# Optimization experiments

Hardware: AMD Instinct MI355X
Metric: run time of the kernel (lower is better)

The kernel has to match this reference:

```python
import jax, jax.numpy as jnp
import numpy as np

EMBED_DIM = 1024
LN_EPS = 1e-5


def _layernorm(x, w, b):
    m = jnp.mean(x, axis=-1, keepdims=True)
    v = jnp.mean(jnp.square(x - m), axis=-1, keepdims=True)
    return (x - m) * jax.lax.rsqrt(v + LN_EPS) * w + b


def _attention(q, k, v, scale):
    # q: [b, sq, d], k/v: [b, sk, d]
    scores = jnp.einsum('bqd,bkd->bqk', q, k) * scale
    probs = jax.nn.softmax(scores, axis=-1)
    return jnp.einsum('bqk,bkd->bqd', probs, v)


def setup_inputs() -> dict:
    key = jax.random.key(0)
    ks = jax.random.split(key, 16)
    B, SQ, SK, D, H = 8, 577, 13271, EMBED_DIM, 4  # H=int(4.0) per source
    return {
        'input_features': jax.random.normal(ks[0], (B, SK, D), jnp.float32),
        'query_feature': jax.random.normal(ks[1], (B, SQ, D), jnp.float32),
        'norm1_w': jax.random.uniform(ks[2], (D,), jnp.float32, 0.5, 1.5),
        'norm1_b': jax.random.normal(ks[3], (D,), jnp.float32) * 0.1,
        'norm2_w': jax.random.uniform(ks[4], (D,), jnp.float32, 0.5, 1.5),
        'norm2_b': jax.random.normal(ks[5], (D,), jnp.float32) * 0.1,
        'norm3_w': jax.random.uniform(ks[6], (D,), jnp.float32, 0.5, 1.5),
        'norm3_b': jax.random.normal(ks[7], (D,), jnp.float32) * 0.1,
        'gamma1': jax.random.uniform(ks[8], (D,), jnp.float32, 0.5, 1.5),
        'gamma2': jax.random.uniform(ks[9], (D,), jnp.float32, 0.5, 1.5),
        'fc1_w': jax.random.normal(ks[10], (H, D), jnp.float32) * (1.0 / np.sqrt(D)),
        'fc1_b': jax.random.normal(ks[11], (H,), jnp.float32) * 0.01,
        'fc2_w': jax.random.normal(ks[12], (D, H), jnp.float32) * (1.0 / np.sqrt(H)),
        'fc2_b': jax.random.normal(ks[13], (D,), jnp.float32) * 0.01,
    }


def reference(input_features, query_feature, norm1_w, norm1_b, norm2_w, norm2_b,
              norm3_w, norm3_b, gamma1, gamma2, fc1_w, fc1_b, fc2_w, fc2_b):
    scale = EMBED_DIM ** (-0.5)
    norm_X = _layernorm(input_features, norm1_w, norm1_b)
    norm_F_L = _layernorm(query_feature, norm2_w, norm2_b)
    # cross attention: query = last-layer feats, key/value = concat of earlier layers
    attended = _attention(norm_F_L, norm_X, norm_X, scale)
    # MLP with exact-erf GELU (torch nn.GELU default), dropout=0 -> identity
    h = jax.nn.gelu(attended @ fc1_w.T + fc1_b, approximate=False)
    cross_attended = h @ fc2_w.T + fc2_b
    norm_cross = _layernorm(cross_attended, norm3_w, norm3_b)
    self_attended = _attention(norm_cross, norm_cross, norm_cross, scale)
    skip_connect = cross_attended + gamma1 * self_attended
    return norm_F_L + gamma2 * skip_connect
```

## Files before the change

### kernel.cpp

```cpp
#include <hip/hip_runtime.h>
#include <hip/hip_bf16.h>
#include <math.h>

typedef unsigned short u16;
typedef __attribute__((ext_vector_type(4))) unsigned short u16x4;
typedef __attribute__((ext_vector_type(8))) __bf16 bf16x8;
typedef __attribute__((ext_vector_type(4))) float fx4;

#define DEV __device__ __forceinline__

DEV u16 f2bf(float f) {
    unsigned u = __float_as_uint(f);
    u += 0x7fffu + ((u >> 16) & 1u);
    return (u16)(u >> 16);
}

DEV void async_load16(const void* g, void* l) {
    __builtin_amdgcn_global_load_lds(
        (const __attribute__((address_space(1))) void*)g,
        (__attribute__((address_space(3))) void*)l, 16, 0, 0);
}

DEV void block_reduce2(float& a, float& b) {
    #pragma unroll
    for (int o = 32; o; o >>= 1) { a += __shfl_xor(a, o); b += __shfl_xor(b, o); }
    __shared__ float sa[4], sb[4];
    const int lane = threadIdx.x & 63, wv = threadIdx.x >> 6;
    if (lane == 0) { sa[wv] = a; sb[wv] = b; }
    __syncthreads();
    a = sa[0] + sa[1] + sa[2] + sa[3];
    b = sb[0] + sb[1] + sb[2] + sb[3];
    __syncthreads();
}

DEV void xcd_swizzle3(int& bx, int& by, int& bz) {
    const int nx = gridDim.x, ny = gridDim.y;
    const int total = nx * ny * gridDim.z;
    const int lin = blockIdx.x + nx * (blockIdx.y + ny * blockIdx.z);
    if (total & 7) { bx = blockIdx.x; by = blockIdx.y; bz = blockIdx.z; return; }
    const int cpx = total >> 3;
    const int swz = (lin & 7) * cpx + (lin >> 3);
    bx = swz % nx;
    const int r = swz / nx;
    by = r % ny;
    bz = r / ny;
}

__global__ __launch_bounds__(256) void ln_k(
    const float* __restrict__ in, int rows_real,
    const float* __restrict__ w, const float* __restrict__ bias,
    u16* __restrict__ out_bf, float* __restrict__ out_f32, float out_scale)
{
    const int r = blockIdx.x, b = blockIdx.y, tid = threadIdx.x;
    const int rows_pad = gridDim.x;
    const size_t orow = ((size_t)b * rows_pad + r) * 1024 + tid * 4;
    if (r >= rows_real) {
        u16x4 z = {0, 0, 0, 0};
        *(u16x4*)&out_bf[orow] = z;
        if (out_f32) { fx4 zf = {0.f, 0.f, 0.f, 0.f}; *(fx4*)&out_f32[orow] = zf; }
        return;
    }
    const size_t irow = ((size_t)b * rows_real + r) * 1024 + tid * 4;
    fx4 x = *(const fx4*)&in[irow];
    float s1 = x.x + x.y + x.z + x.w;
    float s2 = x.x * x.x + x.y * x.y + x.z * x.z + x.w * x.w;
    block_reduce2(s1, s2);
    float m = s1 * (1.0f / 1024.0f);
    float var = s2 * (1.0f / 1024.0f) - m * m;
    float rs = rsqrtf(var + 1e-5f);
    fx4 wv4 = *(const fx4*)&w[tid * 4];
    fx4 bv4 = *(const fx4*)&bias[tid * 4];
    fx4 y;
    y.x = (x.x - m) * rs * wv4.x + bv4.x;
    y.y = (x.y - m) * rs * wv4.y + bv4.y;
    y.z = (x.z - m) * rs * wv4.z + bv4.z;
    y.w = (x.w - m) * rs * wv4.w + bv4.w;
    u16x4 o = { f2bf(y.x * out_scale), f2bf(y.y * out_scale),
                f2bf(y.z * out_scale), f2bf(y.w * out_scale) };
    *(u16x4*)&out_bf[orow] = o;
    if (out_f32) *(fx4*)&out_f32[orow] = y;
}

template<bool ATOMIC>
DEV void gemm_body(
    const u16* __restrict__ Ab, const u16* __restrict__ Bb, float* __restrict__ Cb,
    int k_begin, int iters, int lda, int ldb, int ldc)
{
    __shared__ u16 lA[2][128 * 32];
    __shared__ u16 lB[2][128 * 32];
    const int lane = threadIdx.x & 63, wv = threadIdx.x >> 6;
    const int wm = (wv >> 1) * 64, wn = (wv & 1) * 64;
    const int frow = lane & 15, quad = lane >> 4;

    fx4 acc[4][4];
    #pragma unroll
    for (int i = 0; i < 4; ++i)
        #pragma unroll
        for (int j = 0; j < 4; ++j) { acc[i][j].x = 0; acc[i][j].y = 0; acc[i][j].z = 0; acc[i][j].w = 0; }

    const int c0 = wv * 64 + lane;
    const int r0a = c0 >> 2, s0 = (c0 & 3) * 8;
    const int c1 = 256 + c0;
    const int r1a = c1 >> 2, s1 = (c1 & 3) * 8;

    auto stage = [&](int buf, int it) {
        const int k0 = k_begin + it * 32;
        async_load16(Ab + (size_t)r0a * lda + k0 + s0, &lA[buf][(wv * 64) * 8]);
        async_load16(Ab + (size_t)r1a * lda + k0 + s1, &lA[buf][(256 + wv * 64) * 8]);
        async_load16(Bb + (size_t)r0a * ldb + k0 + s0, &lB[buf][(wv * 64) * 8]);
        async_load16(Bb + (size_t)r1a * ldb + k0 + s1, &lB[buf][(256 + wv * 64) * 8]);
    };

    stage(0, 0);
    __syncthreads();
    int cur = 0;
    for (int it = 0; it < iters; ++it) {
        if (it + 1 < iters) stage(cur ^ 1, it + 1);
        bf16x8 af[4], bfr[4];
        #pragma unroll
        for (int i = 0; i < 4; ++i) {
            af[i]  = *(const bf16x8*)&lA[cur][(wm + i * 16 + frow) * 32 + quad * 8];
            bfr[i] = *(const bf16x8*)&lB[cur][(wn + i * 16 + frow) * 32 + quad * 8];
        }
        #pragma unroll
        for (int mi = 0; mi < 4; ++mi)
            #pragma unroll
            for (int ni = 0; ni < 4; ++ni)
                acc[mi][ni] = __builtin_amdgcn_mfma_f32_16x16x32_bf16(af[mi], bfr[ni], acc[mi][ni], 0, 0, 0);
        __syncthreads();
        cur ^= 1;
    }

    #pragma unroll
    for (int mi = 0; mi < 4; ++mi) {
        #pragma unroll
        for (int r = 0; r < 4; ++r) {
            const int row = wm + mi * 16 + quad * 4 + r;
            #pragma unroll
            for (int ni = 0; ni < 4; ++ni) {
                const int col = wn + ni * 16 + frow;
                if (ATOMIC) atomicAdd(&Cb[(size_t)row * ldc + col], acc[mi][ni][r]);
                else        __builtin_nontemporal_store(acc[mi][ni][r], &Cb[(size_t)row * ldc + col]);
            }
        }
    }
}

template<int NS>
__global__ __launch_bounds__(256) void gemm_bt_sk(
    const u16* __restrict__ A, const u16* __restrict__ B, float* __restrict__ C,
    int iters_per, int lda, int ldb, int ldc, long As, long Bs, long Cs)
{
    int bx, by, bzz;
    xcd_swizzle3(bx, by, bzz);
    const int bz = bzz / NS, sp = bzz % NS;
    const u16* Ab = A + (size_t)bz * As + (size_t)by * 128 * lda;
    const u16* Bb = B + (size_t)bz * Bs + (size_t)bx * 128 * ldb;
    float* Cb = C + (size_t)bz * Cs + (size_t)by * 128 * ldc + (size_t)bx * 128;
    gemm_body<true>(Ab, Bb, Cb, sp * iters_per * 32, iters_per, lda, ldb, ldc);
}

template<bool ATOMIC>
DEV void gemm256_body(
    const u16* __restrict__ A, const u16* __restrict__ B, float* __restrict__ C,
    int k_begin, int NT, int lda, int ldb, int ldc, int bx, int by, int Mreal)
{
    __shared__ u16 lds[2][4][8192];
    const int tid = threadIdx.x;
    const int lane = tid & 63, wid = tid >> 6;
    const int wr = wid >> 2, wc = wid & 3;
    const int frow = lane & 15, quad = lane >> 4;
    const int sw = (frow & 7) << 4;
    const int csrc = ((lane & 7) ^ ((lane >> 3) & 7)) * 8;
    const int by256 = by * 256, bx256 = bx * 256;
    const int mclamp = Mreal - 1;

    fx4 acc[8][4];
    #pragma unroll
    for (int i = 0; i < 8; ++i)
        #pragma unroll
        for (int j = 0; j < 4; ++j) { acc[i][j].x = 0; acc[i][j].y = 0; acc[i][j].z = 0; acc[i][j].w = 0; }

    auto stageA = [&](int buf, int half, int ktile) {
        const int kcol = k_begin + ktile * 64;
        #pragma unroll
        for (int j = 0; j < 2; ++j) {
            int grow = by256 + half * 128 + (wid * 2 + j) * 8 + (lane >> 3);
            if (grow > mclamp) grow = mclamp;
            async_load16(A + (size_t)grow * lda + kcol + csrc,
                         &lds[buf][half][(wid * 2 + j) * 512]);
        }
    };
    auto stageB = [&](int buf, int half, int ktile) {
        const int kcol = k_begin + ktile * 64;
        #pragma unroll
        for (int j = 0; j < 2; ++j) {
            const int grow = bx256 + half * 128 + (wid * 2 + j) * 8 + (lane >> 3);
            async_load16(B + (size_t)grow * ldb + kcol + csrc,
                         &lds[buf][2 + half][(wid * 2 + j) * 512]);
        }
    };

#define DO_PHASE(MQ, NQ, STAGE_STMT, WAITN)                                              \
    {                                                                                    \
        STAGE_STMT;                                                                      \
        __builtin_amdgcn_sched_barrier(0);                                               \
        asm volatile("s_waitcnt vmcnt(" #WAITN ")" ::: "memory");                        \
        __builtin_amdgcn_s_barrier();                                                    \
        __builtin_amdgcn_sched_barrier(0);                                               \
        const char* pa = (const char*)&lds[cur][MQ][0];                                  \
        const char* pb = (const char*)&lds[cur][2 + NQ][0];                              \
        bf16x8 av[4][2], bv[2][2];                                                       \
        _Pragma("unroll")                                                                \
        for (int f = 0; f < 4; ++f) {                                                    \
            const int row = wr * 64 + f * 16 + frow;                                     \
            _Pragma("unroll")                                                            \
            for (int ks = 0; ks < 2; ++ks)                                               \
                av[f][ks] = *(const bf16x8*)(pa + row * 128 + ((((ks * 4 + quad) << 4)) ^ sw)); \
        }                                                                                \
        _Pragma("unroll")                                                                \
        for (int gg = 0; gg < 2; ++gg) {                                                 \
            const int col = wc * 32 + gg * 16 + frow;                                    \
            _Pragma("unroll")                                                            \
            for (int ks = 0; ks < 2; ++ks)                                               \
                bv[gg][ks] = *(const bf16x8*)(pb + col * 128 + ((((ks * 4 + quad) << 4)) ^ sw)); \
        }                                                                                \
        __builtin_amdgcn_s_setprio(1);                                                   \
        _Pragma("unroll")                                                                \
        for (int f = 0; f < 4; ++f)                                                      \
            _Pragma("unroll")                                                            \
            for (int gg = 0; gg < 2; ++gg)                                               \
                _Pragma("unroll")                                                        \
                for (int ks = 0; ks < 2; ++ks)                                           \
                    acc[MQ * 4 + f][NQ * 2 + gg] = __builtin_amdgcn_mfma_f32_16x16x32_bf16( \
                        av[f][ks], bv[gg][ks], acc[MQ * 4 + f][NQ * 2 + gg], 0, 0, 0);   \
        __builtin_amdgcn_s_setprio(0);                                                   \
    }

    stageA(0, 0, 0);
    stageB(0, 0, 0);
    stageB(0, 1, 0);
    stageA(0, 1, 0);
    stageA(1, 0, 1);

    int cur = 0;
    for (int t = 0; t <= NT - 2; ++t) {
        const int nxt = cur ^ 1;
        DO_PHASE(0, 0, stageB(nxt, 0, t + 1), 8)
        DO_PHASE(0, 1, stageB(nxt, 1, t + 1), 8)
        DO_PHASE(1, 0, stageA(nxt, 1, t + 1), 8)
        DO_PHASE(1, 1, if (t + 2 < NT) stageA(cur, 0, t + 2), 8)
        cur = nxt;
    }
    DO_PHASE(0, 0, (void)0, 4)
    DO_PHASE(0, 1, (void)0, 2)
    DO_PHASE(1, 0, (void)0, 0)
    DO_PHASE(1, 1, (void)0, 0)
#undef DO_PHASE

    #pragma unroll
    for (int mf = 0; mf < 8; ++mf) {
        const int rowb = (mf >> 2) * 128 + wr * 64 + (mf & 3) * 16 + quad * 4;
        #pragma unroll
        for (int r = 0; r < 4; ++r) {
            const int grow = by256 + rowb + r;
            if (grow < Mreal) {
                #pragma unroll
                for (int nf = 0; nf < 4; ++nf) {
                    const int gcol = bx256 + (nf >> 1) * 128 + wc * 32 + (nf & 1) * 16 + frow;
                    if (ATOMIC) atomicAdd(&C[(size_t)grow * ldc + gcol], acc[mf][nf][r]);
                    else __builtin_nontemporal_store(acc[mf][nf][r], &C[(size_t)grow * ldc + gcol]);
                }
            }
        }
    }
}

__global__ __launch_bounds__(512, 2) void gemm256_qk(
    const u16* __restrict__ A, const u16* __restrict__ B, float* __restrict__ C,
    int NT, int lda, int ldb, int ldc, long As, long Bs, long Cs, int Mreal)
{
    const int lin = blockIdx.x + gridDim.x * (blockIdx.y + gridDim.y * blockIdx.z);
    const int per_bx = gridDim.y * gridDim.z;
    const int bx = lin / per_bx, rem = lin % per_bx;
    const int by = rem % gridDim.y, bz = rem / gridDim.y;
    gemm256_body<false>(A + (size_t)bz * As, B + (size_t)bz * Bs, C + (size_t)bz * Cs,
                        0, NT, lda, ldb, ldc, bx, by, Mreal);
}

template<int NS>
__global__ __launch_bounds__(512, 2) void gemm256_sk(
    const u16* __restrict__ A, const u16* __restrict__ B, float* __restrict__ C,
    int NT_per, int lda, int ldb, int ldc, long As, long Bs, long Cs, int Mreal)
{
    int bx, by, bzz;
    xcd_swizzle3(bx, by, bzz);
    const int bz = bzz / NS, sp = bzz % NS;
    gemm256_body<true>(A + (size_t)bz * As, B + (size_t)bz * Bs, C + (size_t)bz * Cs,
                       sp * NT_per * 64, NT_per, lda, ldb, ldc, bx, by, Mreal);
}

template<int EPT4>
__global__ __launch_bounds__(256) void softmax_k(
    const float* __restrict__ S, u16* __restrict__ P,
    int n_real, int n_pad, float scale, long Ss, long Ps)
{
    const int tid = threadIdx.x;
    const float* Sr = S + (size_t)blockIdx.y * Ss + (size_t)blockIdx.x * n_pad;
    u16* Pr = P + (size_t)blockIdx.y * Ps + (size_t)blockIdx.x * n_pad;
    fx4 v[EPT4];
    float mx = -INFINITY;
    #pragma unroll
    for (int i = 0; i < EPT4; ++i) {
        const int base = (i * 256 + tid) * 4;
        fx4 s;
        if (base < n_pad) s = *(const fx4*)&Sr[base];
        else { s.x = -INFINITY; s.y = -INFINITY; s.z = -INFINITY; s.w = -INFINITY; }
        s.x = (base + 0 < n_real) ? s.x * scale : -INFINITY;
        s.y = (base + 1 < n_real) ? s.y * scale : -INFINITY;
        s.z = (base + 2 < n_real) ? s.z * scale : -INFINITY;
        s.w = (base + 3 < n_real) ? s.w * scale : -INFINITY;
        v[i] = s;
        mx = fmaxf(mx, fmaxf(fmaxf(s.x, s.y), fmaxf(s.z, s.w)));
    }
    #pragma unroll
    for (int o = 32; o; o >>= 1) mx = fmaxf(mx, __shfl_xor(mx, o));
    __shared__ float sm[4];
    const int lane = tid & 63, wvi = tid >> 6;
    if (lane == 0) sm[wvi] = mx;
    __syncthreads();
    mx = fmaxf(fmaxf(sm[0], sm[1]), fmaxf(sm[2], sm[3]));
    __syncthreads();
    float sum = 0.f;
    #pragma unroll
    for (int i = 0; i < EPT4; ++i) {
        fx4 e;
        e.x = __expf(v[i].x - mx); e.y = __expf(v[i].y - mx);
        e.z = __expf(v[i].z - mx); e.w = __expf(v[i].w - mx);
        v[i] = e;
        sum += e.x + e.y + e.z + e.w;
    }
    #pragma unroll
    for (int o = 32; o; o >>= 1) sum += __shfl_xor(sum, o);
    if (lane == 0) sm[wvi] = sum;
    __syncthreads();
    sum = sm[0] + sm[1] + sm[2] + sm[3];
    const float inv = 1.0f / sum;
    #pragma unroll
    for (int i = 0; i < EPT4; ++i) {
        const int base = (i * 256 + tid) * 4;
        if (base < n_pad) {
            u16x4 o = { f2bf(v[i].x * inv), f2bf(v[i].y * inv),
                        f2bf(v[i].z * inv), f2bf(v[i].w * inv) };
            *(u16x4*)&Pr[base] = o;
        }
    }
}

__global__ __launch_bounds__(256) void transpose_k(
    const u16* __restrict__ in, u16* __restrict__ out,
    int in_rows, int in_cols, long is, long os)
{
    __shared__ u16 t[64][68];
    const int b = blockIdx.z;
    const u16* I = in + (size_t)b * is;
    u16* O = out + (size_t)b * os;
    const int c0 = blockIdx.x * 64, r0 = blockIdx.y * 64;
    const int cx = threadIdx.x & 15, ry = threadIdx.x >> 4;
    u16x4 a[4];
    #pragma unroll
    for (int k = 0; k < 4; ++k)
        a[k] = *(const u16x4*)&I[(size_t)(r0 + 4 * ry + k) * in_cols + c0 + 4 * cx];
    #pragma unroll
    for (int e = 0; e < 4; ++e) {
        u16x4 o = { a[0][e], a[1][e], a[2][e], a[3][e] };
        *(u16x4*)&t[4 * cx + e][4 * ry] = o;
    }
    __syncthreads();
    #pragma unroll
    for (int k = 0; k < 4; ++k) {
        const int oc = 4 * ry + k;
        *(u16x4*)&O[(size_t)(c0 + oc) * in_rows + r0 + 4 * cx] =
            *(const u16x4*)&t[oc][4 * cx];
    }
}

__global__ __launch_bounds__(256) void mlp_ln_k(
    const float* __restrict__ att, const float* __restrict__ w1, const float* __restrict__ b1,
    const float* __restrict__ w2, const float* __restrict__ b2,
    const float* __restrict__ w3, const float* __restrict__ b3,
    float* __restrict__ ca, u16* __restrict__ nc, int rows_real)
{
    const int q = blockIdx.x, b = blockIdx.y, tid = threadIdx.x;
    const size_t row = ((size_t)b * gridDim.x + q) * 1024 + tid * 4;
    if (q >= rows_real) {
        fx4 zf = {0.f, 0.f, 0.f, 0.f}; u16x4 z = {0, 0, 0, 0};
        *(fx4*)&ca[row] = zf;
        *(u16x4*)&nc[row] = z;
        return;
    }
    fx4 x = *(const fx4*)&att[row];
    float p[4];
    #pragma unroll
    for (int j = 0; j < 4; ++j) {
        fx4 wj = *(const fx4*)&w1[j * 1024 + tid * 4];
        p[j] = x.x * wj.x + x.y * wj.y + x.z * wj.z + x.w * wj.w;
        #pragma unroll
        for (int o = 32; o; o >>= 1) p[j] += __shfl_xor(p[j], o);
    }
    __shared__ float sh[4][4];
    const int lane = tid & 63, wvi = tid >> 6;
    if (lane == 0) { sh[wvi][0] = p[0]; sh[wvi][1] = p[1]; sh[wvi][2] = p[2]; sh[wvi][3] = p[3]; }
    __syncthreads();
    float h[4];
    #pragma unroll
    for (int j = 0; j < 4; ++j) {
        float s = sh[0][j] + sh[1][j] + sh[2][j] + sh[3][j] + b1[j];
        h[j] = 0.5f * s * (1.0f + erff(s * 0.70710678118f));
    }
    float v[4]; float s1 = 0.f, s2 = 0.f;
    #pragma unroll
    for (int e = 0; e < 4; ++e) {
        const int d = tid * 4 + e;
        fx4 wd = *(const fx4*)&w2[d * 4];
        float t = h[0] * wd.x + h[1] * wd.y + h[2] * wd.z + h[3] * wd.w + b2[d];
        v[e] = t; s1 += t; s2 += t * t;
    }
    block_reduce2(s1, s2);
    const float m = s1 * (1.0f / 1024.0f);
    const float var = s2 * (1.0f / 1024.0f) - m * m;
    const float rs = rsqrtf(var + 1e-5f);
    fx4 cav = {v[0], v[1], v[2], v[3]};
    *(fx4*)&ca[row] = cav;
    fx4 w3v = *(const fx4*)&w3[tid * 4], b3v = *(const fx4*)&b3[tid * 4];
    u16x4 o = { f2bf((v[0] - m) * rs * w3v.x + b3v.x), f2bf((v[1] - m) * rs * w3v.y + b3v.y),
                f2bf((v[2] - m) * rs * w3v.z + b3v.z), f2bf((v[3] - m) * rs * w3v.w + b3v.w) };
    *(u16x4*)&nc[row] = o;
}

__global__ __launch_bounds__(256) void final_k(
    const float* __restrict__ nF, const float* __restrict__ ca,
    const float* __restrict__ att2, const float* __restrict__ g1,
    const float* __restrict__ g2, float* __restrict__ out, int sq, int sqp)
{
    const int q = blockIdx.x, b = blockIdx.y, tid = threadIdx.x;
    const size_t wrow = ((size_t)b * sqp + q) * 1024 + tid * 4;
    const size_t orow = ((size_t)b * sq + q) * 1024 + tid * 4;
    fx4 nf = *(const fx4*)&nF[wrow];
    fx4 c  = *(const fx4*)&ca[wrow];
    fx4 a2 = *(const fx4*)&att2[wrow];
    fx4 G1 = *(const fx4*)&g1[tid * 4];
    fx4 G2 = *(const fx4*)&g2[tid * 4];
    fx4 r;
    r.x = nf.x + G2.x * (c.x + G1.x * a2.x);
    r.y = nf.y + G2.y * (c.y + G1.y * a2.y);
    r.z = nf.z + G2.z * (c.z + G1.z * a2.z);
    r.w = nf.w + G2.w * (c.w + G1.w * a2.w);
    *(fx4*)&out[orow] = r;
}

extern "C" void kernel_launch(void* const* d_in, const int* in_sizes, int n_in,
                              void* d_out, int out_size, void* d_ws, size_t ws_size,
                              hipStream_t stream) {
    const float* x_in = (const float*)d_in[0];
    const float* q_in = (const float*)d_in[1];
    const float* n1w = (const float*)d_in[2];
    const float* n1b = (const float*)d_in[3];
    const float* n2w = (const float*)d_in[4];
    const float* n2b = (const float*)d_in[5];
    const float* n3w = (const float*)d_in[6];
    const float* n3b = (const float*)d_in[7];
    const float* g1  = (const float*)d_in[8];
    const float* g2  = (const float*)d_in[9];
    const float* w1  = (const float*)d_in[10];
    const float* b1  = (const float*)d_in[11];
    const float* w2  = (const float*)d_in[12];
    const float* b2  = (const float*)d_in[13];
    float* out = (float*)d_out;

    const int B = 8, SQ = 577, SK = 13271, D = 1024;
    const int SQP = 640, SKP = 13312;
    const float scale = 0.03125f;

    char* ws = (char*)d_ws;
    size_t off = 0;
    auto alloc = [&](size_t n) { size_t o = off; off = (off + n + 255) & ~(size_t)255; return o; };
    u16*   Xn   = (u16*)  (ws + alloc((size_t)B * SKP * D * 2));
    u16*   Xt   = (u16*)  (ws + alloc((size_t)B * D * SKP * 2));
    u16*   Qb   = (u16*)  (ws + alloc((size_t)B * SQP * D * 2));
    float* nF   = (float*)(ws + alloc((size_t)B * SQP * D * 4));
    u16*   P    = (u16*)  (ws + alloc((size_t)B * SQP * SKP * 2));
    float* att  = (float*)(ws + alloc((size_t)B * SQP * D * 4));
    float* CA   = (float*)(ws + alloc((size_t)B * SQP * D * 4));
    u16*   NC   = (u16*)  (ws + alloc((size_t)B * SQP * D * 2));
    u16*   NCt  = (u16*)  (ws + alloc((size_t)B * D * SQP * 2));
    float* S2   = (float*)(ws + alloc((size_t)B * SQP * SQP * 4));
    u16*   P2   = (u16*)  (ws + alloc((size_t)B * SQP * SQP * 2));
    float* att2 = (float*)(ws + alloc((size_t)B * SQP * D * 4));
    const size_t perS1 = (size_t)SQP * SKP * 4;
    size_t room = (ws_size > off) ? (ws_size - off) / perS1 : 1;
    int g = (int)(room < 1 ? 1 : (room > 8 ? 8 : room));
    float* S1 = (float*)(ws + off);
    (void)in_sizes; (void)n_in; (void)out_size;

    ln_k<<<dim3(SKP, B), 256, 0, stream>>>(x_in, SK, n1w, n1b, Xn, nullptr, 1.0f);
    ln_k<<<dim3(SQP, B), 256, 0, stream>>>(q_in, SQ, n2w, n2b, Qb, nF, scale);

    transpose_k<<<dim3(D / 64, SKP / 64, B), 256, 0, stream>>>(
        Xn, Xt, SKP, D, (long)SKP * D, (long)SKP * D);

    for (int b = 0; b < B; b += g) {
        const int nb = (B - b) < g ? (B - b) : g;
        gemm256_qk<<<dim3(SKP / 256, 3, nb), 512, 0, stream>>>(
            Qb + (size_t)b * SQP * D, Xn + (size_t)b * SKP * D, S1,
            D / 64, D, D, SKP, (long)SQP * D, (long)SKP * D, (long)SQP * SKP, SQP);
        softmax_k<13><<<dim3(SQP, nb), 256, 0, stream>>>(
            S1, P + (size_t)b * SQP * SKP, SK, SKP, 1.0f,
            (long)SQP * SKP, (long)SQP * SKP);
    }

    hipMemsetAsync(att, 0, (size_t)B * SQP * D * 4, stream);
    gemm256_sk<8><<<dim3(D / 256, 3, B * 8), 512, 0, stream>>>(
        P, Xt, att, (SKP / 64) / 8, SKP, SKP, D,
        (long)SQP * SKP, (long)D * SKP, (long)SQP * D, SQP);

    mlp_ln_k<<<dim3(SQP, B), 256, 0, stream>>>(att, w1, b1, w2, b2, n3w, n3b, CA, NC, SQ);

    transpose_k<<<dim3(D / 64, SQP / 64, B), 256, 0, stream>>>(
        NC, NCt, SQP, D, (long)SQP * D, (long)SQP * D);
    hipMemsetAsync(S2, 0, (size_t)B * SQP * SQP * 4, stream);
    gemm_bt_sk<2><<<dim3(SQP / 128, SQP / 128, B * 2), 256, 0, stream>>>(
        NC, NC, S2, 16, D, D, SQP,
        (long)SQP * D, (long)SQP * D, (long)SQP * SQP);
    softmax_k<1><<<dim3(SQP, B), 256, 0, stream>>>(
        S2, P2, SQ, SQP, scale, (long)SQP * SQP, (long)SQP * SQP);
    hipMemsetAsync(att2, 0, (size_t)B * SQP * D * 4, stream);
    gemm_bt_sk<4><<<dim3(D / 128, SQP / 128, B * 4), 256, 0, stream>>>(
        P2, NCt, att2, 5, SQP, SQP, D,
        (long)SQP * SQP, (long)D * SQP, (long)SQP * D);

    final_k<<<dim3(SQ, B), 256, 0, stream>>>(nF, CA, att2, g1, g2, out, SQ, SQP);
}
```

Before: 1.321 ms.

## Use one wave per row in layernorm, plain GEMM stores, smaller S1 batch group

Rewrites the layernorm kernel so each 64-lane wave handles a full 1024-wide row with shuffle reductions, replacing the block-wide LDS reduction and its barriers. GEMM epilogues switch from nontemporal stores to normal stores, so the score matrices can stay in cache for the following softmax. The batch group size for the QK/softmax loop is capped at 4 instead of 8, shrinking the S1 working set so it is more likely to fit in cache, at the cost of more kernel launches.

```diff
diff --git a/kernel.cpp b/kernel.cpp
--- a/kernel.cpp
+++ b/kernel.cpp
@@ -46,39 +46,52 @@
     bz = r / ny;
 }
 
-__global__ __launch_bounds__(256) void ln_k(
-    const float* __restrict__ in, int rows_real,
+__global__ __launch_bounds__(256) void ln_wave_k(
+    const float* __restrict__ in, int rows_real, int rows_pad,
     const float* __restrict__ w, const float* __restrict__ bias,
     u16* __restrict__ out_bf, float* __restrict__ out_f32, float out_scale)
 {
-    const int r = blockIdx.x, b = blockIdx.y, tid = threadIdx.x;
-    const int rows_pad = gridDim.x;
-    const size_t orow = ((size_t)b * rows_pad + r) * 1024 + tid * 4;
+    const int wv = threadIdx.x >> 6, lane = threadIdx.x & 63;
+    const int r = blockIdx.x * 4 + wv, b = blockIdx.y;
+    const size_t orow = ((size_t)b * rows_pad + r) * 1024 + lane * 4;
     if (r >= rows_real) {
         u16x4 z = {0, 0, 0, 0};
-        *(u16x4*)&out_bf[orow] = z;
-        if (out_f32) { fx4 zf = {0.f, 0.f, 0.f, 0.f}; *(fx4*)&out_f32[orow] = zf; }
+        fx4 zf = {0.f, 0.f, 0.f, 0.f};
+        #pragma unroll
+        for (int c = 0; c < 4; ++c) {
+            *(u16x4*)&out_bf[orow + c * 256] = z;
+            if (out_f32) *(fx4*)&out_f32[orow + c * 256] = zf;
+        }
         return;
     }
-    const size_t irow = ((size_t)b * rows_real + r) * 1024 + tid * 4;
-    fx4 x = *(const fx4*)&in[irow];
-    float s1 = x.x + x.y + x.z + x.w;
-    float s2 = x.x * x.x + x.y * x.y + x.z * x.z + x.w * x.w;
-    block_reduce2(s1, s2);
-    float m = s1 * (1.0f / 1024.0f);
-    float var = s2 * (1.0f / 1024.0f) - m * m;
-    float rs = rsqrtf(var + 1e-5f);
-    fx4 wv4 = *(const fx4*)&w[tid * 4];
-    fx4 bv4 = *(const fx4*)&bias[tid * 4];
-    fx4 y;
-    y.x = (x.x - m) * rs * wv4.x + bv4.x;
-    y.y = (x.y - m) * rs * wv4.y + bv4.y;
-    y.z = (x.z - m) * rs * wv4.z + bv4.z;
-    y.w = (x.w - m) * rs * wv4.w + bv4.w;
-    u16x4 o = { f2bf(y.x * out_scale), f2bf(y.y * out_scale),
-                f2bf(y.z * out_scale), f2bf(y.w * out_scale) };
-    *(u16x4*)&out_bf[orow] = o;
-    if (out_f32) *(fx4*)&out_f32[orow] = y;
+    const size_t irow = ((size_t)b * rows_real + r) * 1024 + lane * 4;
+    fx4 x[4];
+    float s1 = 0.f, s2 = 0.f;
+    #pragma unroll
+    for (int c = 0; c < 4; ++c) {
+        x[c] = *(const fx4*)&in[irow + c * 256];
+        s1 += x[c].x + x[c].y + x[c].z + x[c].w;
+        s2 += x[c].x * x[c].x + x[c].y * x[c].y + x[c].z * x[c].z + x[c].w * x[c].w;
+    }
+    #pragma unroll
+    for (int o = 32; o; o >>= 1) { s1 += __shfl_xor(s1, o); s2 += __shfl_xor(s2, o); }
+    const float m = s1 * (1.0f / 1024.0f);
+    const float var = s2 * (1.0f / 1024.0f) - m * m;
+    const float rs = rsqrtf(var + 1e-5f);
+    #pragma unroll
+    for (int c = 0; c < 4; ++c) {
+        fx4 wv4 = *(const fx4*)&w[c * 256 + lane * 4];
+        fx4 bv4 = *(const fx4*)&bias[c * 256 + lane * 4];
+        fx4 y;
+        y.x = (x[c].x - m) * rs * wv4.x + bv4.x;
+        y.y = (x[c].y - m) * rs * wv4.y + bv4.y;
+        y.z = (x[c].z - m) * rs * wv4.z + bv4.z;
+        y.w = (x[c].w - m) * rs * wv4.w + bv4.w;
+        u16x4 o = { f2bf(y.x * out_scale), f2bf(y.y * out_scale),
+                    f2bf(y.z * out_scale), f2bf(y.w * out_scale) };
+        *(u16x4*)&out_bf[orow + c * 256] = o;
+        if (out_f32) *(fx4*)&out_f32[orow + c * 256] = y;
+    }
 }
 
 template<bool ATOMIC>
@@ -140,7 +153,7 @@
             for (int ni = 0; ni < 4; ++ni) {
                 const int col = wn + ni * 16 + frow;
                 if (ATOMIC) atomicAdd(&Cb[(size_t)row * ldc + col], acc[mi][ni][r]);
-                else        __builtin_nontemporal_store(acc[mi][ni][r], &Cb[(size_t)row * ldc + col]);
+                else        Cb[(size_t)row * ldc + col] = acc[mi][ni][r];
             }
         }
     }
@@ -269,7 +282,7 @@
                 for (int nf = 0; nf < 4; ++nf) {
                     const int gcol = bx256 + (nf >> 1) * 128 + wc * 32 + (nf & 1) * 16 + frow;
                     if (ATOMIC) atomicAdd(&C[(size_t)grow * ldc + gcol], acc[mf][nf][r]);
-                    else __builtin_nontemporal_store(acc[mf][nf][r], &C[(size_t)grow * ldc + gcol]);
+                    else C[(size_t)grow * ldc + gcol] = acc[mf][nf][r];
                 }
             }
         }
@@ -499,12 +512,12 @@
     float* att2 = (float*)(ws + alloc((size_t)B * SQP * D * 4));
     const size_t perS1 = (size_t)SQP * SKP * 4;
     size_t room = (ws_size > off) ? (ws_size - off) / perS1 : 1;
-    int g = (int)(room < 1 ? 1 : (room > 8 ? 8 : room));
+    int g = (int)(room < 1 ? 1 : (room > 4 ? 4 : room));
     float* S1 = (float*)(ws + off);
     (void)in_sizes; (void)n_in; (void)out_size;
 
-    ln_k<<<dim3(SKP, B), 256, 0, stream>>>(x_in, SK, n1w, n1b, Xn, nullptr, 1.0f);
-    ln_k<<<dim3(SQP, B), 256, 0, stream>>>(q_in, SQ, n2w, n2b, Qb, nF, scale);
+    ln_wave_k<<<dim3(SKP / 4, B), 256, 0, stream>>>(x_in, SK, SKP, n1w, n1b, Xn, nullptr, 1.0f);
+    ln_wave_k<<<dim3(SQP / 4, B), 256, 0, stream>>>(q_in, SQ, SQP, n2w, n2b, Qb, nF, scale);
 
     transpose_k<<<dim3(D / 64, SKP / 64, B), 256, 0, stream>>>(
         Xn, Xt, SKP, D, (long)SKP * D, (long)SKP * D);
```

Result: no change. 1.344 ms (+1.8%).
